# Kernel tuning notes

Hardware: AMD Instinct MI355X
Metric: run time of the kernel (lower is better)

The kernel has to match this reference:

```python
import jax, jax.numpy as jnp
import numpy as np

B, S, N, F, G, H = 32, 512, 64, 16, 64, 256  # batch, seq, nodes, in_feat, gcn_hidden, gru_hidden
EPS = 1e-5


def setup_inputs() -> dict:
    key = jax.random.key(0)
    ks = jax.random.split(key, 24)
    def rn(k, shape, scale):
        return jax.random.normal(k, shape, dtype=jnp.float32) * scale
    inp = {
        'x': jax.random.normal(ks[0], (B, S, N, F), dtype=jnp.float32),
        'adj': jax.random.uniform(ks[1], (N, N), dtype=jnp.float32) / N,
        # GCN layer 0: input_dim -> G ; layer 1: G -> G
        'W0': rn(ks[2], (F, G), 1.0 / np.sqrt(F)),
        'b0': jnp.zeros((G,), jnp.float32),
        'W1': rn(ks[3], (G, G), 1.0 / np.sqrt(G)),
        'b1': jnp.zeros((G,), jnp.float32),
        # BatchNorm1d(num_nodes), eval mode (running stats)
        'bn_g': 1.0 + rn(ks[4], (N,), 0.1),
        'bn_b': rn(ks[5], (N,), 0.1),
        'bn_m': rn(ks[6], (N,), 0.1),
        'bn_v': 0.5 + jax.random.uniform(ks[7], (N,), dtype=jnp.float32),
        # GRU layer 0 (input N*G -> H), gate order r,z,n as in torch
        'Wih0': rn(ks[8], (3 * H, N * G), 1.0 / np.sqrt(N * G)),
        'Whh0': rn(ks[9], (3 * H, H), 1.0 / np.sqrt(H)),
        'bih0': rn(ks[10], (3 * H,), 0.02),
        'bhh0': rn(ks[11], (3 * H,), 0.02),
        # GRU layer 1 (H -> H)
        'Wih1': rn(ks[12], (3 * H, H), 1.0 / np.sqrt(H)),
        'Whh1': rn(ks[13], (3 * H, H), 1.0 / np.sqrt(H)),
        'bih1': rn(ks[14], (3 * H,), 0.02),
        'bhh1': rn(ks[15], (3 * H,), 0.02),
        # head: fc1 H -> H//2, fc2 H//2 -> N*output_dim (output_dim=1)
        'fc1_w': rn(ks[16], (H, H // 2), 1.0 / np.sqrt(H)),
        'fc1_b': jnp.zeros((H // 2,), jnp.float32),
        'fc2_w': rn(ks[17], (H // 2, N), 1.0 / np.sqrt(H // 2)),
        'fc2_b': jnp.zeros((N,), jnp.float32),
    }
    return inp


def _gru_layer(xs, Wih, Whh, bih, bhh):
    # xs: [B, S, D] -> ys: [B, S, H]; torch GRU cell math, gate order r,z,n
    b, s, _ = xs.shape
    h0 = jnp.zeros((b, Whh.shape[1]), xs.dtype)
    def step(h, x_t):
        gi = x_t @ Wih.T + bih
        gh = h @ Whh.T + bhh
        ir, iz, inn = jnp.split(gi, 3, axis=-1)
        hr, hz, hn = jnp.split(gh, 3, axis=-1)
        r = jax.nn.sigmoid(ir + hr)
        z = jax.nn.sigmoid(iz + hz)
        n = jnp.tanh(inn + r * hn)
        h_new = (1.0 - z) * n + z * h
        return h_new, h_new
    _, ys = jax.lax.scan(step, h0, jnp.swapaxes(xs, 0, 1))  # scan over time
    return jnp.swapaxes(ys, 0, 1)


def reference(x, adj, W0, b0, W1, b1, bn_g, bn_b, bn_m, bn_v,
              Wih0, Whh0, bih0, bhh0, Wih1, Whh1, bih1, bhh1,
              fc1_w, fc1_b, fc2_w, fc2_b):
    b, s, n, _ = x.shape
    g = W0.shape[1]
    # GCN layer 0 over all timesteps at once: adj @ h @ W + b, then ReLU
    h = jax.nn.relu(jnp.einsum('uv,bsvf,fg->bsug', adj, x, W0) + b0)
    # BatchNorm1d over the node channel (eval mode); dropout = identity (eval)
    inv = jax.lax.rsqrt(bn_v + EPS)
    h = (h - bn_m[:, None]) * (inv * bn_g)[:, None] + bn_b[:, None]
    # GCN layer 1 (last layer: no BN/dropout)
    h = jax.nn.relu(jnp.einsum('uv,bsvf,fg->bsug', adj, h, W1) + b1)
    # flatten nodes*features -> GRU temporal input [B, S, N*G]
    seq = h.reshape(b, s, n * g)
    y = _gru_layer(seq, Wih0, Whh0, bih0, bhh0)
    y = _gru_layer(y, Wih1, Whh1, bih1, bhh1)  # inter-layer dropout = identity (eval)
    last = y[:, -1, :]                         # [B, H]
    o = jax.nn.relu(last @ fc1_w + fc1_b)
    o = o @ fc2_w + fc2_b                      # [B, N*output_dim]
    return o.reshape(b, n, 1)
```

## Files before the change

### kernel.cpp

```cpp
#include <hip/hip_runtime.h>
#include <hip/hip_bf16.h>


#define EPS_BN 1e-5f

typedef float f32x4 __attribute__((ext_vector_type(4)));
typedef unsigned u32x4v __attribute__((ext_vector_type(4)));

#define GRU_BARRIER() do {                       \
    asm volatile("" ::: "memory");               \
    asm volatile("s_waitcnt lgkmcnt(0)");        \
    __builtin_amdgcn_s_barrier();                \
    asm volatile("" ::: "memory");               \
  } while (0)

__global__ void k_split16(const float* __restrict__ src,
                          _Float16* __restrict__ hi, _Float16* __restrict__ lo,
                          int n) {
  int i = blockIdx.x * 256 + threadIdx.x;
  if (i >= n) return;
  float v = src[i];
  _Float16 h = (_Float16)v;
  hi[i] = h;
  lo[i] = (_Float16)(v - (float)h);
}

__global__ void k_pack_frag(const float* __restrict__ whh, uint4* __restrict__ wp) {
  int tid = blockIdx.x * 256 + threadIdx.x;
  if (tid >= 24576) return;
  int l = tid & 63;
  int rest = tid >> 6;
  int ks = rest & 7; rest >>= 3;
  int nt = rest % 6;
  int w  = rest / 6;
  int n  = 16 * w + 128 * nt + (l & 15);
  int kb = ks * 32 + (l >> 4) * 8;
  const float* src = whh + (size_t)n * 256 + kb;
  unsigned dw[4];
#pragma unroll
  for (int d = 0; d < 4; ++d) {
    unsigned short lo = __builtin_bit_cast(unsigned short, (_Float16)src[2 * d]);
    unsigned short hi = __builtin_bit_cast(unsigned short, (_Float16)src[2 * d + 1]);
    dw[d] = (unsigned)lo | ((unsigned)hi << 16);
  }
  wp[tid] = make_uint4(dw[0], dw[1], dw[2], dw[3]);
}

__global__ __launch_bounds__(256) void k_gcn(
    const float* __restrict__ x, const float* __restrict__ adj,
    const float* __restrict__ W0, const float* __restrict__ b0,
    const float* __restrict__ W1, const float* __restrict__ b1,
    const float* __restrict__ bn_g, const float* __restrict__ bn_b,
    const float* __restrict__ bn_m, const float* __restrict__ bn_v,
    _Float16* __restrict__ seqh, _Float16* __restrict__ seql, int base)
{
  __shared__ float As[4096];
  __shared__ float Xs[1024];
  __shared__ float Hs[4096];
  __shared__ float Qs[4096];
  __shared__ float bnm_s[64], bns_s[64], bnb_s[64];

  const int t = threadIdx.x;
  const int lane = t & 63;
  const int w = t >> 6;
  const int m = base + blockIdx.x;

  {
    const float4* a4 = (const float4*)adj;
    float4* s4 = (float4*)As;
#pragma unroll
    for (int p = 0; p < 4; ++p) {
      const int idx = t + 256 * p;
      const float4 av = a4[idx];
      s4[idx] = av;
      const int u = idx >> 4, v4 = (idx & 15) * 4;
      Qs[(v4 + 0) * 64 + u] = av.x;
      Qs[(v4 + 1) * 64 + u] = av.y;
      Qs[(v4 + 2) * 64 + u] = av.z;
      Qs[(v4 + 3) * 64 + u] = av.w;
    }
    ((float4*)Xs)[t] = ((const float4*)(x + (size_t)m * 1024))[t];
  }
  if (t < 64) {
    bns_s[t] = rsqrtf(bn_v[t] + EPS_BN) * bn_g[t];
    bnm_s[t] = bn_m[t];
    bnb_s[t] = bn_b[t];
  }
  float w0r[16];
#pragma unroll
  for (int f = 0; f < 16; ++f) w0r[f] = W0[f * 64 + lane];
  const float b0v = b0[lane], b1v = b1[lane];
  __syncthreads();

  float axr[4] = {0.f, 0.f, 0.f, 0.f};
  const int f0 = w * 4;
#pragma unroll
  for (int v = 0; v < 64; ++v) {
    const float a_vu = Qs[v * 64 + lane];
    const float4 xv = *(const float4*)&Xs[v * 16 + f0];
    axr[0] = fmaf(a_vu, xv.x, axr[0]);
    axr[1] = fmaf(a_vu, xv.y, axr[1]);
    axr[2] = fmaf(a_vu, xv.z, axr[2]);
    axr[3] = fmaf(a_vu, xv.w, axr[3]);
  }
  __syncthreads();
#pragma unroll
  for (int j = 0; j < 4; ++j) Xs[lane * 16 + f0 + j] = axr[j];
  __syncthreads();

#pragma unroll
  for (int uu = 0; uu < 16; ++uu) {
    const int u = w * 16 + uu;
    float acc = 0.f;
#pragma unroll
    for (int f = 0; f < 16; ++f) acc += Xs[u * 16 + f] * w0r[f];
    float h1 = fmaxf(acc + b0v, 0.f);
    h1 = (h1 - bnm_s[u]) * bns_s[u] + bnb_s[u];
    Hs[u * 64 + lane] = h1;
  }
  __syncthreads();

  float w1r[64];
#pragma unroll
  for (int f = 0; f < 64; ++f) w1r[f] = W1[f * 64 + lane];
#pragma unroll
  for (int vv = 0; vv < 16; ++vv) {
    int v = w * 16 + vv;
    float acc = 0.f;
#pragma unroll
    for (int f = 0; f < 64; ++f) acc += Hs[v * 64 + f] * w1r[f];
    Qs[v * 64 + lane] = acc;
  }
  __syncthreads();
  float q[64];
#pragma unroll
  for (int v = 0; v < 64; ++v) q[v] = Qs[v * 64 + lane];
  _Float16* oh = seqh + (size_t)blockIdx.x * 4096;
  _Float16* ol = seql + (size_t)blockIdx.x * 4096;
#pragma unroll
  for (int uu = 0; uu < 16; ++uu) {
    int u = w * 16 + uu;
    float acc = 0.f;
#pragma unroll
    for (int v = 0; v < 64; ++v) acc += As[u * 64 + v] * q[v];
    float val = fmaxf(acc + b1v, 0.f);
    _Float16 hv = (_Float16)val;
    oh[u * 64 + lane] = hv;
    ol[u * 64 + lane] = (_Float16)(val - (float)hv);
  }
}

#define MFMA_VV(c, a, b) asm volatile("v_mfma_f32_16x16x32_f16 %0, %1, %2, %0" \
                                      : "+v"(c) : "v"(a), "v"(b))

__global__ __launch_bounds__(256, 2) void k_gemm_lds(
    const _Float16* __restrict__ Ah, const _Float16* __restrict__ Al,
    const _Float16* __restrict__ Bh, const _Float16* __restrict__ Bl,
    const float* __restrict__ bias,
    float* __restrict__ C,
    int K, int mBlocks)
{
  __shared__ u32x4v frag[2][32][64];
  const int bid = blockIdx.x;
  const int mb = bid % mBlocks;
  const int nb = bid / mBlocks;
  const int t = threadIdx.x;
  const int w = t >> 6, l = t & 63;
  const int m0 = mb * 128, n0 = nb * 128;
  const int mh = w >> 1, nh = w & 1;
  const int row = l & 15;

  const _Float16* src[8];
#pragma unroll
  for (int s = 0; s < 8; ++s) {
    const int gs = w * 8 + s;
    const bool isB = gs >= 16;
    const int tile = (gs & 15) >> 1;
    const int hl = gs & 1;
    const _Float16* base = isB ? (hl ? Bl : Bh) : (hl ? Al : Ah);
    const int r = (isB ? n0 : m0) + 16 * tile + row;
    src[s] = base + (size_t)r * K + ((l >> 4) * 8);
  }

  f32x4 acc[4][4] = {};
  u32x4v st[8];

#pragma unroll
  for (int s = 0; s < 8; ++s) st[s] = *(const u32x4v*)(src[s]);
#pragma unroll
  for (int s = 0; s < 8; ++s) frag[0][w * 8 + s][l] = st[s];
  __syncthreads();

  int cur = 0;
#pragma unroll 1
  for (int kt = 0; kt < K; kt += 32) {
    const bool more = (kt + 32) < K;
    if (more) {
#pragma unroll
      for (int s = 0; s < 8; ++s) st[s] = *(const u32x4v*)(src[s] + kt + 32);
    }

    u32x4v afh[4], afl[4], bfh[4], bfl[4];
#pragma unroll
    for (int i = 0; i < 4; ++i) {
      afh[i] = frag[cur][2 * (mh * 4 + i)][l];
      afl[i] = frag[cur][2 * (mh * 4 + i) + 1][l];
      bfh[i] = frag[cur][16 + 2 * (nh * 4 + i)][l];
      bfl[i] = frag[cur][16 + 2 * (nh * 4 + i) + 1][l];
    }

#pragma unroll
    for (int mi = 0; mi < 4; ++mi)
#pragma unroll
      for (int ni = 0; ni < 4; ++ni)
        MFMA_VV(acc[mi][ni], afh[mi], bfh[ni]);
#pragma unroll
    for (int mi = 0; mi < 4; ++mi)
#pragma unroll
      for (int ni = 0; ni < 4; ++ni)
        MFMA_VV(acc[mi][ni], afl[mi], bfh[ni]);
#pragma unroll
    for (int mi = 0; mi < 4; ++mi)
#pragma unroll
      for (int ni = 0; ni < 4; ++ni)
        MFMA_VV(acc[mi][ni], afh[mi], bfl[ni]);

    if (more) {
#pragma unroll
      for (int s = 0; s < 8; ++s) frag[cur ^ 1][w * 8 + s][l] = st[s];
    }
    __syncthreads();
    cur ^= 1;
  }

  asm volatile("s_nop 7\n\ts_nop 7");

  const int m0w = m0 + mh * 64;
  const int n0w = n0 + nh * 64;
  const int r4 = (l >> 4) * 4;
#pragma unroll
  for (int ni = 0; ni < 4; ++ni) {
    const float bv = bias[n0w + 16 * ni + row];
#pragma unroll
    for (int mi = 0; mi < 4; ++mi) {
      float* cp = C + (size_t)(m0w + 16 * mi + r4) * 768 + n0w + 16 * ni + row;
      cp[0]    = acc[mi][ni].x + bv;
      cp[768]  = acc[mi][ni].y + bv;
      cp[1536] = acc[mi][ni].z + bv;
      cp[2304] = acc[mi][ni].w + bv;
    }
  }
}

#define MFMA_A(c, a, b) asm volatile("v_mfma_f32_16x16x32_f16 %0, %1, %2, %0" \
                                     : "+v"(c) : "v"(a), "a"(b))

template <bool WF16, bool LASTONLY>
__global__ __launch_bounds__(512, 2) void k_gru(
    const float* __restrict__ gi,
    const uint4* __restrict__ wp,
    const float* __restrict__ bhh,
    float* __restrict__ ys,
    _Float16* __restrict__ ysh,
    _Float16* __restrict__ ysl)
{
  const int b = blockIdx.x;
  const int t = threadIdx.x;
  const int w = t >> 6;
  const int l = t & 63;

  __shared__ __align__(16) _Float16 h2[2][256];

  const u32x4v* wp4 = (const u32x4v*)wp;
  const int wbase = w * 6;

#define LBK(nt, ks) const u32x4v b##nt##_##ks = wp4[(((wbase + nt) * 8 + ks) << 6) + l];
#define LBNT(nt) LBK(nt,0) LBK(nt,1) LBK(nt,2) LBK(nt,3) \
                 LBK(nt,4) LBK(nt,5) LBK(nt,6) LBK(nt,7)
  LBNT(0) LBNT(1) LBNT(2) LBNT(3) LBNT(4) LBNT(5)
#undef LBNT
#undef LBK

  const int half = (l >> 4) & 1;
  const int j = 16 * w + (l & 15) + 128 * half;
  const bool act = (l < 32);
  float br = 0.f, bz = 0.f, bn = 0.f;
  float hold = 0.f;
  if (act) { br = bhh[j]; bz = bhh[256 + j]; bn = bhh[512 + j]; }
  if (t < 256) { h2[0][t] = (_Float16)0.f; h2[1][t] = (_Float16)0.f; }
  __syncthreads();

  const float* gib = gi + (size_t)b * 512 * 768;
  const char* h2c = (const char*)h2;
  const int g16 = (l >> 4) * 16;
  int cur = 0;

#pragma unroll 1
  for (int step = 0; step < 512; ++step) {
    float ir = 0.f, iz = 0.f, inn = 0.f;
    if (act) {
      const float* g = gib + (size_t)step * 768;
      ir = g[j]; iz = g[256 + j]; inn = g[512 + j];
    }

    f32x4 c0 = {0.f,0.f,0.f,0.f}, c1 = c0, c2 = c0, c3 = c0, c4 = c0, c5 = c0;

#define DOT_KS(ks) { \
    const u32x4v a = *(const u32x4v*)(h2c + cur * 512 + (ks) * 64 + g16); \
    MFMA_A(c0, a, b0_##ks); MFMA_A(c1, a, b1_##ks); MFMA_A(c2, a, b2_##ks); \
    MFMA_A(c3, a, b3_##ks); MFMA_A(c4, a, b4_##ks); MFMA_A(c5, a, b5_##ks); }
    DOT_KS(0) DOT_KS(1) DOT_KS(2) DOT_KS(3)
    DOT_KS(4) DOT_KS(5) DOT_KS(6) DOT_KS(7)
#undef DOT_KS
    asm volatile("s_nop 7\n\ts_nop 7");

    if (act) {
      const float cr = half ? c1.x : c0.x;
      const float cz = half ? c3.x : c2.x;
      const float cn = half ? c5.x : c4.x;
      const float r = __builtin_amdgcn_rcpf(1.f + __expf(-(ir + cr + br)));
      const float z = __builtin_amdgcn_rcpf(1.f + __expf(-(iz + cz + bz)));
      const float e2 = __expf(2.f * (inn + r * (cn + bn)));
      const float n = 1.f - 2.f * __builtin_amdgcn_rcpf(e2 + 1.f);
      hold = (1.f - z) * n + z * hold;
      h2[cur ^ 1][j] = (_Float16)hold;
      const size_t rowi = (size_t)b * 512 + step;
      if (WF16) {
        const _Float16 hh = (_Float16)hold;
        ysh[rowi * 256 + j] = hh;
        ysl[rowi * 256 + j] = (_Float16)(hold - (float)hh);
      }
      if (LASTONLY) {
        if (step == 511) ys[rowi * 256 + j] = hold;
      }
    }
    GRU_BARRIER();
    cur ^= 1;
  }
}

__global__ __launch_bounds__(128) void k_head(
    const float* __restrict__ ys1,
    const float* __restrict__ fc1w, const float* __restrict__ fc1b,
    const float* __restrict__ fc2w, const float* __restrict__ fc2b,
    float* __restrict__ out)
{
  __shared__ float last[256];
  __shared__ float o1[128];
  const int b = blockIdx.x, t = threadIdx.x;
  const float* src = ys1 + (size_t)(b * 512 + 511) * 256;
  last[t] = src[t];
  last[128 + t] = src[128 + t];
  __syncthreads();
  float acc = fc1b[t];
#pragma unroll 8
  for (int k = 0; k < 256; ++k) acc += last[k] * fc1w[k * 128 + t];
  o1[t] = fmaxf(acc, 0.f);
  __syncthreads();
  if (t < 64) {
    float acc2 = fc2b[t];
#pragma unroll 8
    for (int i = 0; i < 128; ++i) acc2 += o1[i] * fc2w[i * 64 + t];
    out[b * 64 + t] = acc2;
  }
}

extern "C" void kernel_launch(void* const* d_in, const int* in_sizes, int n_in,
                              void* d_out, int out_size, void* d_ws, size_t ws_size,
                              hipStream_t stream)
{
  const float* x    = (const float*)d_in[0];
  const float* adj  = (const float*)d_in[1];
  const float* W0   = (const float*)d_in[2];
  const float* b0   = (const float*)d_in[3];
  const float* W1   = (const float*)d_in[4];
  const float* b1   = (const float*)d_in[5];
  const float* bng  = (const float*)d_in[6];
  const float* bnbb = (const float*)d_in[7];
  const float* bnm  = (const float*)d_in[8];
  const float* bnv  = (const float*)d_in[9];
  const float* Wih0 = (const float*)d_in[10];
  const float* Whh0 = (const float*)d_in[11];
  const float* bih0 = (const float*)d_in[12];
  const float* bhh0 = (const float*)d_in[13];
  const float* Wih1 = (const float*)d_in[14];
  const float* Whh1 = (const float*)d_in[15];
  const float* bih1 = (const float*)d_in[16];
  const float* bhh1 = (const float*)d_in[17];
  const float* fc1w = (const float*)d_in[18];
  const float* fc1b = (const float*)d_in[19];
  const float* fc2w = (const float*)d_in[20];
  const float* fc2b = (const float*)d_in[21];
  float* out = (float*)d_out;

  float* ws = (float*)d_ws;
  const size_t fixed = (size_t)16384 * 768 + (size_t)16384 * 256
                     + 2 * ((size_t)16384 * 128)
                     + 2 * 98304
                     + 2 * ((size_t)768 * 4096 / 2)
                     + 2 * ((size_t)768 * 256 / 2);
  int CHUNK = 16384;
  while (CHUNK > 128 && ((size_t)CHUNK * 4096 + fixed) * 4 > ws_size) CHUNK >>= 1;

  size_t off = 0;
  _Float16* seqh = (_Float16*)(ws + off); off += (size_t)CHUNK * 2048;
  _Float16* seql = (_Float16*)(ws + off); off += (size_t)CHUNK * 2048;
  float* gi      = ws + off; off += (size_t)16384 * 768;
  float* ys1     = ws + off; off += (size_t)16384 * 256;
  _Float16* ysh  = (_Float16*)(ws + off); off += (size_t)16384 * 128;
  _Float16* ysl  = (_Float16*)(ws + off); off += (size_t)16384 * 128;
  uint4* wp0     = (uint4*)(ws + off); off += 98304;
  uint4* wp1     = (uint4*)(ws + off); off += 98304;
  _Float16* bh0  = (_Float16*)(ws + off); off += (size_t)768 * 2048;
  _Float16* bl0  = (_Float16*)(ws + off); off += (size_t)768 * 2048;
  _Float16* bh1  = (_Float16*)(ws + off); off += (size_t)768 * 128;
  _Float16* bl1  = (_Float16*)(ws + off); off += (size_t)768 * 128;

  k_pack_frag<<<96, 256, 0, stream>>>(Whh0, wp0);
  k_pack_frag<<<96, 256, 0, stream>>>(Whh1, wp1);
  k_split16<<<(3145728 + 255) / 256, 256, 0, stream>>>(Wih0, bh0, bl0, 3145728);
  k_split16<<<(196608 + 255) / 256, 256, 0, stream>>>(Wih1, bh1, bl1, 196608);

  const int nChunks = 16384 / CHUNK;
  for (int ci = 0; ci < nChunks; ++ci) {
    const int base = ci * CHUNK;
    k_gcn<<<CHUNK, 256, 0, stream>>>(x, adj, W0, b0, W1, b1, bng, bnbb, bnm, bnv,
                                     seqh, seql, base);
    const int mB = CHUNK / 128;
    k_gemm_lds<<<mB * 6, 256, 0, stream>>>(seqh, seql, bh0, bl0, bih0,
                                           gi + (size_t)base * 768, 4096, mB);
  }
  k_gru<true, false><<<32, 512, 0, stream>>>(gi, wp0, bhh0, nullptr, ysh, ysl);
  k_gemm_lds<<<128 * 6, 256, 0, stream>>>(ysh, ysl, bh1, bl1, bih1, gi, 256, 128);
  k_gru<false, true><<<32, 512, 0, stream>>>(gi, wp1, bhh1, ys1, nullptr, nullptr);
  k_head<<<32, 128, 0, stream>>>(ys1, fc1w, fc1b, fc2w, fc2b, out);
}
```

Measured before the change: 2.412 ms.

## Move GCN layer-1 matmuls onto split-fp16 MFMA with prepacked adj/W1 fragments

Replaces the scalar FP32 loops for H@W1 and adj@Q in the GCN kernel with v_mfma_f32_16x16x32_f16 using a hi/lo fp16 split (three MFMA products) to keep near-fp32 accuracy. A new pack kernel pre-splits adj and W1 into MFMA fragment layout in workspace. Intermediates are stored in padded fp16 hi/lo LDS tiles. The aim is to cut the per-timestep FMA cost of the GCN stage, in exchange for a small accuracy change from dropping the lo×lo term and from quantising intermediates.

```diff
diff --git a/kernel.cpp b/kernel.cpp
--- a/kernel.cpp
+++ b/kernel.cpp
@@ -13,6 +13,11 @@
     __builtin_amdgcn_s_barrier();                \
     asm volatile("" ::: "memory");               \
   } while (0)
+
+#define MFMA_VV(c, a, b) asm volatile("v_mfma_f32_16x16x32_f16 %0, %1, %2, %0" \
+                                      : "+v"(c) : "v"(a), "v"(b))
+#define MFMA_A(c, a, b) asm volatile("v_mfma_f32_16x16x32_f16 %0, %1, %2, %0" \
+                                     : "+v"(c) : "v"(a), "a"(b))
 
 __global__ void k_split16(const float* __restrict__ src,
                           _Float16* __restrict__ hi, _Float16* __restrict__ lo,
@@ -46,18 +51,66 @@
   wp[tid] = make_uint4(dw[0], dw[1], dw[2], dw[3]);
 }
 
+__global__ void k_pack_gcn(const float* __restrict__ adj, const float* __restrict__ W1,
+                           uint4* __restrict__ adjFh, uint4* __restrict__ adjFl,
+                           uint4* __restrict__ w1Fh, uint4* __restrict__ w1Fl) {
+  int tid = blockIdx.x * 256 + threadIdx.x;
+  if (tid >= 1024) return;
+  int l = tid & 63;
+  int fi = (tid >> 6) & 7;
+  bool isW1 = tid >= 512;
+  int tile = fi >> 1, ks = fi & 1;
+  int rc = tile * 16 + (l & 15);
+  int kb = ks * 32 + (l >> 4) * 8;
+  unsigned hdw[4], ldw[4];
+#pragma unroll
+  for (int d2 = 0; d2 < 4; ++d2) {
+    unsigned short hv2[2], lv2[2];
+#pragma unroll
+    for (int e = 0; e < 2; ++e) {
+      int k = kb + 2 * d2 + e;
+      float v = isW1 ? W1[k * 64 + rc] : adj[rc * 64 + k];
+      _Float16 hv = (_Float16)v;
+      _Float16 lv = (_Float16)(v - (float)hv);
+      hv2[e] = __builtin_bit_cast(unsigned short, hv);
+      lv2[e] = __builtin_bit_cast(unsigned short, lv);
+    }
+    hdw[d2] = (unsigned)hv2[0] | ((unsigned)hv2[1] << 16);
+    ldw[d2] = (unsigned)lv2[0] | ((unsigned)lv2[1] << 16);
+  }
+  uint4 hq = make_uint4(hdw[0], hdw[1], hdw[2], hdw[3]);
+  uint4 lq = make_uint4(ldw[0], ldw[1], ldw[2], ldw[3]);
+  if (isW1) { w1Fh[fi * 64 + l] = hq; w1Fl[fi * 64 + l] = lq; }
+  else      { adjFh[fi * 64 + l] = hq; adjFl[fi * 64 + l] = lq; }
+}
+
+static __device__ __forceinline__ unsigned pk2(float a, float b, float& ra, float& rb) {
+  _Float16 ha = (_Float16)a, hb = (_Float16)b;
+  ra = a - (float)ha; rb = b - (float)hb;
+  return (unsigned)__builtin_bit_cast(unsigned short, ha) |
+         ((unsigned)__builtin_bit_cast(unsigned short, hb) << 16);
+}
+static __device__ __forceinline__ unsigned pk2r(float a, float b) {
+  _Float16 ha = (_Float16)a, hb = (_Float16)b;
+  return (unsigned)__builtin_bit_cast(unsigned short, ha) |
+         ((unsigned)__builtin_bit_cast(unsigned short, hb) << 16);
+}
+
 __global__ __launch_bounds__(256) void k_gcn(
-    const float* __restrict__ x, const float* __restrict__ adj,
+    const float* __restrict__ x,
+    const float* __restrict__ adj,
     const float* __restrict__ W0, const float* __restrict__ b0,
-    const float* __restrict__ W1, const float* __restrict__ b1,
+    const uint4* __restrict__ adjFh, const uint4* __restrict__ adjFl,
+    const uint4* __restrict__ w1Fh, const uint4* __restrict__ w1Fl,
+    const float* __restrict__ b1,
     const float* __restrict__ bn_g, const float* __restrict__ bn_b,
     const float* __restrict__ bn_m, const float* __restrict__ bn_v,
     _Float16* __restrict__ seqh, _Float16* __restrict__ seql, int base)
 {
-  __shared__ float As[4096];
+  __shared__ float AsT[4096];
   __shared__ float Xs[1024];
-  __shared__ float Hs[4096];
-  __shared__ float Qs[4096];
+  __shared__ __align__(16) _Float16 Hsh[64 * 72], Hsl[64 * 72];
+  __shared__ __align__(16) _Float16 Qth[64 * 72], Qtl[64 * 72];
   __shared__ float bnm_s[64], bns_s[64], bnb_s[64];
 
   const int t = threadIdx.x;
@@ -67,17 +120,15 @@
 
   {
     const float4* a4 = (const float4*)adj;
-    float4* s4 = (float4*)As;
 #pragma unroll
     for (int p = 0; p < 4; ++p) {
       const int idx = t + 256 * p;
       const float4 av = a4[idx];
-      s4[idx] = av;
       const int u = idx >> 4, v4 = (idx & 15) * 4;
-      Qs[(v4 + 0) * 64 + u] = av.x;
-      Qs[(v4 + 1) * 64 + u] = av.y;
-      Qs[(v4 + 2) * 64 + u] = av.z;
-      Qs[(v4 + 3) * 64 + u] = av.w;
+      AsT[(v4 + 0) * 64 + u] = av.x;
+      AsT[(v4 + 1) * 64 + u] = av.y;
+      AsT[(v4 + 2) * 64 + u] = av.z;
+      AsT[(v4 + 3) * 64 + u] = av.w;
     }
     ((float4*)Xs)[t] = ((const float4*)(x + (size_t)m * 1024))[t];
   }
@@ -89,14 +140,14 @@
   float w0r[16];
 #pragma unroll
   for (int f = 0; f < 16; ++f) w0r[f] = W0[f * 64 + lane];
-  const float b0v = b0[lane], b1v = b1[lane];
+  const float b0v = b0[lane];
   __syncthreads();
 
   float axr[4] = {0.f, 0.f, 0.f, 0.f};
   const int f0 = w * 4;
 #pragma unroll
   for (int v = 0; v < 64; ++v) {
-    const float a_vu = Qs[v * 64 + lane];
+    const float a_vu = AsT[v * 64 + lane];
     const float4 xv = *(const float4*)&Xs[v * 16 + f0];
     axr[0] = fmaf(a_vu, xv.x, axr[0]);
     axr[1] = fmaf(a_vu, xv.y, axr[1]);
@@ -116,42 +167,103 @@
     for (int f = 0; f < 16; ++f) acc += Xs[u * 16 + f] * w0r[f];
     float h1 = fmaxf(acc + b0v, 0.f);
     h1 = (h1 - bnm_s[u]) * bns_s[u] + bnb_s[u];
-    Hs[u * 64 + lane] = h1;
-  }
-  __syncthreads();
-
-  float w1r[64];
-#pragma unroll
-  for (int f = 0; f < 64; ++f) w1r[f] = W1[f * 64 + lane];
-#pragma unroll
-  for (int vv = 0; vv < 16; ++vv) {
-    int v = w * 16 + vv;
-    float acc = 0.f;
-#pragma unroll
-    for (int f = 0; f < 64; ++f) acc += Hs[v * 64 + f] * w1r[f];
-    Qs[v * 64 + lane] = acc;
-  }
-  __syncthreads();
-  float q[64];
-#pragma unroll
-  for (int v = 0; v < 64; ++v) q[v] = Qs[v * 64 + lane];
-  _Float16* oh = seqh + (size_t)blockIdx.x * 4096;
-  _Float16* ol = seql + (size_t)blockIdx.x * 4096;
-#pragma unroll
-  for (int uu = 0; uu < 16; ++uu) {
-    int u = w * 16 + uu;
-    float acc = 0.f;
-#pragma unroll
-    for (int v = 0; v < 64; ++v) acc += As[u * 64 + v] * q[v];
-    float val = fmaxf(acc + b1v, 0.f);
-    _Float16 hv = (_Float16)val;
-    oh[u * 64 + lane] = hv;
-    ol[u * 64 + lane] = (_Float16)(val - (float)hv);
-  }
-}
-
-#define MFMA_VV(c, a, b) asm volatile("v_mfma_f32_16x16x32_f16 %0, %1, %2, %0" \
-                                      : "+v"(c) : "v"(a), "v"(b))
+    const _Float16 hh = (_Float16)h1;
+    Hsh[u * 72 + lane] = hh;
+    Hsl[u * 72 + lane] = (_Float16)(h1 - (float)hh);
+  }
+  __syncthreads();
+
+  {
+    const int rb = (16 * w + (lane & 15)) * 72 + (lane >> 4) * 8;
+    const u32x4v ah0 = *(const u32x4v*)&Hsh[rb];
+    const u32x4v ah1 = *(const u32x4v*)&Hsh[rb + 32];
+    const u32x4v al0 = *(const u32x4v*)&Hsl[rb];
+    const u32x4v al1 = *(const u32x4v*)&Hsl[rb + 32];
+    u32x4v bh[4][2], bl[4][2];
+#pragma unroll
+    for (int gt = 0; gt < 4; ++gt)
+#pragma unroll
+      for (int ks = 0; ks < 2; ++ks) {
+        bh[gt][ks] = *(const u32x4v*)&w1Fh[(gt * 2 + ks) * 64 + lane];
+        bl[gt][ks] = *(const u32x4v*)&w1Fl[(gt * 2 + ks) * 64 + lane];
+      }
+    f32x4 qa[4] = {};
+#pragma unroll
+    for (int gt = 0; gt < 4; ++gt) MFMA_VV(qa[gt], ah0, bh[gt][0]);
+#pragma unroll
+    for (int gt = 0; gt < 4; ++gt) MFMA_VV(qa[gt], ah1, bh[gt][1]);
+#pragma unroll
+    for (int gt = 0; gt < 4; ++gt) MFMA_VV(qa[gt], al0, bh[gt][0]);
+#pragma unroll
+    for (int gt = 0; gt < 4; ++gt) MFMA_VV(qa[gt], al1, bh[gt][1]);
+#pragma unroll
+    for (int gt = 0; gt < 4; ++gt) MFMA_VV(qa[gt], ah0, bl[gt][0]);
+#pragma unroll
+    for (int gt = 0; gt < 4; ++gt) MFMA_VV(qa[gt], ah1, bl[gt][1]);
+    asm volatile("s_nop 7\n\ts_nop 7");
+#pragma unroll
+    for (int gt = 0; gt < 4; ++gt) {
+      const int g = 16 * gt + (lane & 15);
+      float r0, r1, r2, r3;
+      uint2 uh, ul;
+      uh.x = pk2(qa[gt].x, qa[gt].y, r0, r1);
+      uh.y = pk2(qa[gt].z, qa[gt].w, r2, r3);
+      ul.x = pk2r(r0, r1);
+      ul.y = pk2r(r2, r3);
+      *(uint2*)&Qth[g * 72 + 16 * w + (lane >> 4) * 4] = uh;
+      *(uint2*)&Qtl[g * 72 + 16 * w + (lane >> 4) * 4] = ul;
+    }
+  }
+  __syncthreads();
+
+  {
+    u32x4v aah[2], aal[2];
+#pragma unroll
+    for (int ks = 0; ks < 2; ++ks) {
+      aah[ks] = *(const u32x4v*)&adjFh[(w * 2 + ks) * 64 + lane];
+      aal[ks] = *(const u32x4v*)&adjFl[(w * 2 + ks) * 64 + lane];
+    }
+    u32x4v qbh[4][2], qbl[4][2];
+#pragma unroll
+    for (int gt = 0; gt < 4; ++gt)
+#pragma unroll
+      for (int ks = 0; ks < 2; ++ks) {
+        const int rb3 = (16 * gt + (lane & 15)) * 72 + ks * 32 + (lane >> 4) * 8;
+        qbh[gt][ks] = *(const u32x4v*)&Qth[rb3];
+        qbl[gt][ks] = *(const u32x4v*)&Qtl[rb3];
+      }
+    f32x4 oa[4] = {};
+#pragma unroll
+    for (int gt = 0; gt < 4; ++gt) MFMA_VV(oa[gt], aah[0], qbh[gt][0]);
+#pragma unroll
+    for (int gt = 0; gt < 4; ++gt) MFMA_VV(oa[gt], aah[1], qbh[gt][1]);
+#pragma unroll
+    for (int gt = 0; gt < 4; ++gt) MFMA_VV(oa[gt], aal[0], qbh[gt][0]);
+#pragma unroll
+    for (int gt = 0; gt < 4; ++gt) MFMA_VV(oa[gt], aal[1], qbh[gt][1]);
+#pragma unroll
+    for (int gt = 0; gt < 4; ++gt) MFMA_VV(oa[gt], aah[0], qbl[gt][0]);
+#pragma unroll
+    for (int gt = 0; gt < 4; ++gt) MFMA_VV(oa[gt], aah[1], qbl[gt][1]);
+    asm volatile("s_nop 7\n\ts_nop 7");
+
+    _Float16* oh = seqh + (size_t)blockIdx.x * 4096;
+    _Float16* ol = seql + (size_t)blockIdx.x * 4096;
+    const int ub = 16 * w + (lane >> 4) * 4;
+#pragma unroll
+    for (int gt = 0; gt < 4; ++gt) {
+      const int g = 16 * gt + (lane & 15);
+      const float bv = b1[g];
+#pragma unroll
+      for (int q = 0; q < 4; ++q) {
+        const float val = fmaxf(oa[gt][q] + bv, 0.f);
+        const _Float16 hv = (_Float16)val;
+        oh[(ub + q) * 64 + g] = hv;
+        ol[(ub + q) * 64 + g] = (_Float16)(val - (float)hv);
+      }
+    }
+  }
+}
 
 __global__ __launch_bounds__(256, 2) void k_gemm_lds(
     const _Float16* __restrict__ Ah, const _Float16* __restrict__ Al,
@@ -251,9 +363,6 @@
     }
   }
 }
-
-#define MFMA_A(c, a, b) asm volatile("v_mfma_f32_16x16x32_f16 %0, %1, %2, %0" \
-                                     : "+v"(c) : "v"(a), "a"(b))
 
 template <bool WF16, bool LASTONLY>
 __global__ __launch_bounds__(512, 2) void k_gru(
@@ -398,7 +507,8 @@
                      + 2 * ((size_t)16384 * 128)
                      + 2 * 98304
                      + 2 * ((size_t)768 * 4096 / 2)
-                     + 2 * ((size_t)768 * 256 / 2);
+                     + 2 * ((size_t)768 * 256 / 2)
+                     + 4 * 2048;
   int CHUNK = 16384;
   while (CHUNK > 128 && ((size_t)CHUNK * 4096 + fixed) * 4 > ws_size) CHUNK >>= 1;
 
@@ -415,17 +525,22 @@
   _Float16* bl0  = (_Float16*)(ws + off); off += (size_t)768 * 2048;
   _Float16* bh1  = (_Float16*)(ws + off); off += (size_t)768 * 128;
   _Float16* bl1  = (_Float16*)(ws + off); off += (size_t)768 * 128;
+  uint4* adjFh   = (uint4*)(ws + off); off += 2048;
+  uint4* adjFl   = (uint4*)(ws + off); off += 2048;
+  uint4* w1Fh    = (uint4*)(ws + off); off += 2048;
+  uint4* w1Fl    = (uint4*)(ws + off); off += 2048;
 
   k_pack_frag<<<96, 256, 0, stream>>>(Whh0, wp0);
   k_pack_frag<<<96, 256, 0, stream>>>(Whh1, wp1);
+  k_pack_gcn<<<4, 256, 0, stream>>>(adj, W1, adjFh, adjFl, w1Fh, w1Fl);
   k_split16<<<(3145728 + 255) / 256, 256, 0, stream>>>(Wih0, bh0, bl0, 3145728);
   k_split16<<<(196608 + 255) / 256, 256, 0, stream>>>(Wih1, bh1, bl1, 196608);
 
   const int nChunks = 16384 / CHUNK;
   for (int ci = 0; ci < nChunks; ++ci) {
     const int base = ci * CHUNK;
-    k_gcn<<<CHUNK, 256, 0, stream>>>(x, adj, W0, b0, W1, b1, bng, bnbb, bnm, bnv,
-                                     seqh, seql, base);
+    k_gcn<<<CHUNK, 256, 0, stream>>>(x, adj, W0, b0, adjFh, adjFl, w1Fh, w1Fl,
+                                     b1, bng, bnbb, bnm, bnv, seqh, seql, base);
     const int mB = CHUNK / 128;
     k_gemm_lds<<<mB * 6, 256, 0, stream>>>(seqh, seql, bh0, bl0, bih0,
                                            gi + (size_t)base * 768, 4096, mB);
```

Result: faster. 2.173 ms (-9.9%).
